# Optimization experiments

Hardware: AMD Instinct MI355X
Metric: run time of the kernel (lower is better)

The kernel has to match this reference:

```python
import jax, jax.numpy as jnp
import numpy as np

NUM_GRAPHS = 512

def setup_inputs() -> dict:
    key = jax.random.key(0)
    ks = jax.random.split(key, 16)
    N, E, F_IN, D = 50000, 800000, 128, 64
    x = jax.random.normal(ks[0], (N, F_IN), dtype=jnp.float32)
    edge_index = jax.random.randint(ks[1], (2, E), 0, N, dtype=jnp.int32)
    batch_index = jnp.sort(jax.random.randint(ks[2], (N,), 0, NUM_GRAPHS, dtype=jnp.int32))
    def lin(k, fin, fout):
        s = 1.0 / np.sqrt(fin)
        return jax.random.uniform(k, (fin, fout), jnp.float32, -s, s)
    return {
        "x": x, "edge_index": edge_index, "batch_index": batch_index,
        "W0": lin(ks[3], F_IN, D), "b0": jnp.zeros((D,), jnp.float32),
        "W1": lin(ks[4], D, D), "b1": jnp.zeros((D,), jnp.float32),
        "W2": lin(ks[5], D, D), "b2": jnp.zeros((D,), jnp.float32),
        "W3": lin(ks[6], D, D), "b3": jnp.zeros((D,), jnp.float32),
        "Wout": lin(ks[7], 2 * D, 1), "bout": jnp.zeros((1,), jnp.float32),
    }

def _gcn_edges(edge_index, N):
    # add self-loops and compute symmetric normalization D^-1/2 (A+I) D^-1/2
    loops = jnp.arange(N, dtype=edge_index.dtype)
    row = jnp.concatenate([edge_index[0], loops])  # source
    col = jnp.concatenate([edge_index[1], loops])  # target
    deg = jax.ops.segment_sum(jnp.ones_like(col, dtype=jnp.float32), col, num_segments=N)
    dinv = jnp.where(deg > 0, jax.lax.rsqrt(deg), 0.0)
    norm = dinv[row] * dinv[col]  # [E+N]
    return row, col, norm

def _gcn_conv(h, row, col, norm, W, b, N):
    h = h @ W                                   # [N, D] linear transform first
    msg = h[row] * norm[:, None]                # gather + scale
    out = jax.ops.segment_sum(msg, col, num_segments=N)  # scatter-add
    return out + b

def reference(x, edge_index, batch_index, W0, b0, W1, b1, W2, b2, W3, b3, Wout, bout):
    N = x.shape[0]
    row, col, norm = _gcn_edges(edge_index, N)
    h = jnp.tanh(_gcn_conv(x, row, col, norm, W0, b0, N))
    h = jnp.tanh(_gcn_conv(h, row, col, norm, W1, b1, N))
    h = jnp.tanh(_gcn_conv(h, row, col, norm, W2, b2, N))
    h = jnp.tanh(_gcn_conv(h, row, col, norm, W3, b3, N))
    gmax = jax.ops.segment_max(h, batch_index, num_segments=NUM_GRAPHS)
    gmax = jnp.where(jnp.isfinite(gmax), gmax, 0.0)  # empty segments -> 0
    gsum = jax.ops.segment_sum(h, batch_index, num_segments=NUM_GRAPHS)
    cnt = jax.ops.segment_sum(jnp.ones((N,), jnp.float32), batch_index, num_segments=NUM_GRAPHS)
    gmean = gsum / jnp.maximum(cnt, 1.0)[:, None]
    hidden = jnp.concatenate([gmax, gmean], axis=1)   # [G, 2D]
    out = hidden @ Wout + bout                        # [G, 1]
    return out, hidden
```

## Files before the change

### kernel.cpp

```cpp
#include <hip/hip_runtime.h>
#include <hip/hip_fp16.h>
#include <math.h>

#define CAP 64
typedef unsigned short ushort_t;
typedef unsigned int uint_t;

__device__ inline float4 f4add(float4 a, float4 b) {
    return make_float4(a.x + b.x, a.y + b.y, a.z + b.z, a.w + b.w);
}

__device__ inline float4 h4tof4(uint2 u) {
    __half2 lo = *reinterpret_cast<__half2*>(&u.x);
    __half2 hi = *reinterpret_cast<__half2*>(&u.y);
    float2 a = __half22float2(lo);
    float2 b = __half22float2(hi);
    return make_float4(a.x, a.y, b.x, b.y);
}

__device__ inline uint_t packh2(float a, float b) {
    __half2 h = __floats2half2_rn(a, b);
    return *reinterpret_cast<uint_t*>(&h);
}

__global__ __launch_bounds__(256) void k_scatter2(const int* __restrict__ row,
                                                  const int* __restrict__ col, int E, int N,
                                                  int* __restrict__ deg, ushort_t* __restrict__ csr) {
    const int part = blockIdx.x & 7;
    const int slot = blockIdx.x >> 3;
    const int nslots = gridDim.x >> 3;
    const int lo = (int)((long long)N * part / 8);
    const int hi = (int)((long long)N * (part + 1) / 8);
    const int nq = E >> 2;
    for (int t = slot * blockDim.x + threadIdx.x; t < nq; t += nslots * blockDim.x) {
        int4 c = ((const int4*)col)[t];
        int4 r = ((const int4*)row)[t];
        if (c.x >= lo && c.x < hi) { int d = atomicAdd(&deg[c.x], 1); if (d < CAP) csr[((size_t)c.x << 6) + d] = (ushort_t)r.x; }
        if (c.y >= lo && c.y < hi) { int d = atomicAdd(&deg[c.y], 1); if (d < CAP) csr[((size_t)c.y << 6) + d] = (ushort_t)r.y; }
        if (c.z >= lo && c.z < hi) { int d = atomicAdd(&deg[c.z], 1); if (d < CAP) csr[((size_t)c.z << 6) + d] = (ushort_t)r.z; }
        if (c.w >= lo && c.w < hi) { int d = atomicAdd(&deg[c.w], 1); if (d < CAP) csr[((size_t)c.w << 6) + d] = (ushort_t)r.w; }
    }
    if (blockIdx.x == 0) {
        for (int e = (nq << 2) + threadIdx.x; e < E; e += blockDim.x) {
            int c = col[e];
            int d = atomicAdd(&deg[c], 1);
            if (d < CAP) csr[((size_t)c << 6) + d] = (ushort_t)row[e];
        }
    }
}

template <int K>
__global__ __launch_bounds__(256) void k_gemm(const float* __restrict__ X,
                                              const float* __restrict__ W,
                                              const int* __restrict__ deg,
                                              ushort_t* __restrict__ Gbh, int N) {
    __shared__ __align__(16) float Wl[32 * 64];
    __shared__ __align__(16) float Xl[64 * 36];

    const int tid = threadIdx.x;
    const int wave = tid >> 6, lane = tid & 63;
    const int d8 = lane & 7, ns = lane >> 3;
    const int n0 = wave * 16 + ns, n1 = n0 + 8;

    const int base = blockIdx.x * 64;
    if (base >= N) return;
    const int tile_n = min(64, N - base);

    float4 a0l = {0,0,0,0}, a0h = {0,0,0,0}, a1l = {0,0,0,0}, a1h = {0,0,0,0};

    for (int kh = 0; kh < K / 32; kh++) {
        __syncthreads();
        for (int i = tid; i < 512; i += 256)
            ((float4*)Wl)[i] = ((const float4*)(W + kh * 2048))[i];
        for (int idx = tid; idx < 512; idx += 256) {
            int n = idx >> 3, q = idx & 7;
            float4 v = {0,0,0,0};
            if (n < tile_n) v = ((const float4*)(X + (size_t)(base + n) * K + kh * 32))[q];
            ((float4*)(Xl + n * 36))[q] = v;
        }
        __syncthreads();

        const float4* xq0 = (const float4*)(Xl + n0 * 36);
        const float4* xq1 = (const float4*)(Xl + n1 * 36);
        const float* wcol = Wl + d8 * 8;
#pragma unroll
        for (int kq = 0; kq < 8; kq++) {
            const float4 x4a = xq0[kq];
            const float4 x4b = xq1[kq];
            const float xs0[4] = {x4a.x, x4a.y, x4a.z, x4a.w};
            const float xs1[4] = {x4b.x, x4b.y, x4b.z, x4b.w};
#pragma unroll
            for (int j = 0; j < 4; j++) {
                const int k = kq * 4 + j;
                const float4 wa = *(const float4*)(wcol + k * 64);
                const float4 wb = *(const float4*)(wcol + k * 64 + 4);
                const float xa = xs0[j];
                const float xb = xs1[j];
                a0l.x = fmaf(xa, wa.x, a0l.x); a0l.y = fmaf(xa, wa.y, a0l.y);
                a0l.z = fmaf(xa, wa.z, a0l.z); a0l.w = fmaf(xa, wa.w, a0l.w);
                a0h.x = fmaf(xa, wb.x, a0h.x); a0h.y = fmaf(xa, wb.y, a0h.y);
                a0h.z = fmaf(xa, wb.z, a0h.z); a0h.w = fmaf(xa, wb.w, a0h.w);
                a1l.x = fmaf(xb, wa.x, a1l.x); a1l.y = fmaf(xb, wa.y, a1l.y);
                a1l.z = fmaf(xb, wa.z, a1l.z); a1l.w = fmaf(xb, wa.w, a1l.w);
                a1h.x = fmaf(xb, wb.x, a1h.x); a1h.y = fmaf(xb, wb.y, a1h.y);
                a1h.z = fmaf(xb, wb.z, a1h.z); a1h.w = fmaf(xb, wb.w, a1h.w);
            }
        }
    }

    int gn0 = base + n0, gn1 = base + n1;
    if (gn0 < N) {
        float s = rsqrtf((float)(deg[gn0] + 1));
        uint4 o;
        o.x = packh2(a0l.x * s, a0l.y * s);
        o.y = packh2(a0l.z * s, a0l.w * s);
        o.z = packh2(a0h.x * s, a0h.y * s);
        o.w = packh2(a0h.z * s, a0h.w * s);
        ((uint4*)(Gbh + (size_t)gn0 * 64))[d8] = o;
    }
    if (gn1 < N) {
        float s = rsqrtf((float)(deg[gn1] + 1));
        uint4 o;
        o.x = packh2(a1l.x * s, a1l.y * s);
        o.y = packh2(a1l.z * s, a1l.w * s);
        o.z = packh2(a1h.x * s, a1h.y * s);
        o.w = packh2(a1h.z * s, a1h.w * s);
        ((uint4*)(Gbh + (size_t)gn1 * 64))[d8] = o;
    }
}

__global__ __launch_bounds__(256) void k_agg(const ushort_t* __restrict__ Gbh,
                                             const int* __restrict__ deg,
                                             const ushort_t* __restrict__ csr,
                                             const float* __restrict__ bias,
                                             float* __restrict__ H, int N) {
    const int tid = threadIdx.x;
    const int wave = tid >> 6, lane = tid & 63;
    const int s = lane >> 4;
    const int q = lane & 15;
    const int n = blockIdx.x * 16 + wave * 4 + s;
    const bool alive = (n < N);

    int cnt = 0;
    if (alive) { cnt = deg[n]; if (cnt > CAP) cnt = CAP; }
    const ushort_t* rowp = csr + ((size_t)(alive ? n : 0) << 6);

    uint4 ia = {0,0,0,0}, ib = {0,0,0,0}, ic = {0,0,0,0}, idd = {0,0,0,0};
    if (cnt > 0)  ia  = *(const uint4*)(rowp);
    if (cnt > 8)  ib  = *(const uint4*)(rowp + 8);
    if (cnt > 16) ic  = *(const uint4*)(rowp + 16);
    if (cnt > 24) idd = *(const uint4*)(rowp + 24);

    float4 acc = {0.f, 0.f, 0.f, 0.f};
    if (alive) acc = h4tof4(((const uint2*)(Gbh + (size_t)n * 64))[q]);

    const uint_t iw[16] = {ia.x, ia.y, ia.z, ia.w, ib.x, ib.y, ib.z, ib.w,
                           ic.x, ic.y, ic.z, ic.w, idd.x, idd.y, idd.z, idd.w};

#pragma unroll
    for (int h = 0; h < 2; h++) {
        const int base = h * 16;
        uint2 hv[16];
#pragma unroll
        for (int m = 0; m < 8; m++) {
            const uint_t u = iw[h * 8 + m];
            const int j0 = u & 0xffff, j1 = u >> 16;
            uint2 a = {0u, 0u}, b = {0u, 0u};
            if (base + 2 * m < cnt)     a = ((const uint2*)(Gbh + (size_t)j0 * 64))[q];
            if (base + 2 * m + 1 < cnt) b = ((const uint2*)(Gbh + (size_t)j1 * 64))[q];
            hv[2 * m] = a;
            hv[2 * m + 1] = b;
        }
        float4 t0 = f4add(h4tof4(hv[0]),  h4tof4(hv[1]));
        float4 t1 = f4add(h4tof4(hv[2]),  h4tof4(hv[3]));
        float4 t2 = f4add(h4tof4(hv[4]),  h4tof4(hv[5]));
        float4 t3 = f4add(h4tof4(hv[6]),  h4tof4(hv[7]));
        float4 t4 = f4add(h4tof4(hv[8]),  h4tof4(hv[9]));
        float4 t5 = f4add(h4tof4(hv[10]), h4tof4(hv[11]));
        float4 t6 = f4add(h4tof4(hv[12]), h4tof4(hv[13]));
        float4 t7 = f4add(h4tof4(hv[14]), h4tof4(hv[15]));
        float4 u0 = f4add(t0, t1), u1 = f4add(t2, t3);
        float4 u2 = f4add(t4, t5), u3 = f4add(t6, t7);
        acc = f4add(acc, f4add(f4add(u0, u1), f4add(u2, u3)));
    }

    for (int i = 32; i < cnt; i += 2) {
        const uint_t u = *(const uint_t*)(rowp + i);
        const int j0 = u & 0xffff;
        acc = f4add(acc, h4tof4(((const uint2*)(Gbh + (size_t)j0 * 64))[q]));
        if (i + 1 < cnt) {
            const int j1 = u >> 16;
            acc = f4add(acc, h4tof4(((const uint2*)(Gbh + (size_t)j1 * 64))[q]));
        }
    }

    if (alive) {
        float dinv = rsqrtf((float)(cnt + 1));
        float4 b4 = ((const float4*)bias)[q];
        float4 r;
        r.x = tanhf(fmaf(acc.x, dinv, b4.x));
        r.y = tanhf(fmaf(acc.y, dinv, b4.y));
        r.z = tanhf(fmaf(acc.z, dinv, b4.z));
        r.w = tanhf(fmaf(acc.w, dinv, b4.w));
        ((float4*)(H + (size_t)n * 64))[q] = r;
    }
}

__global__ __launch_bounds__(256) void k_pool(const float* __restrict__ H,
                                              const int* __restrict__ batch, int N, int Gn,
                                              const float* __restrict__ Wout,
                                              const float* __restrict__ bout,
                                              float* __restrict__ out,
                                              float* __restrict__ hidden) {
    __shared__ float lm[4][64];
    __shared__ float ls[4][64];
    const int g = blockIdx.x;
    if (g >= Gn) return;
    const int tid = threadIdx.x;
    const int w = tid >> 6, lane = tid & 63;

    int lo = 0, hi = N;
    while (lo < hi) { int m = (lo + hi) >> 1; if (batch[m] < g) lo = m + 1; else hi = m; }
    const int s = lo;
    hi = N;
    while (lo < hi) { int m = (lo + hi) >> 1; if (batch[m] < g + 1) lo = m + 1; else hi = m; }
    const int c = lo - s;
    const int e = s + c;

    float m0 = -INFINITY, m1 = -INFINITY, m2 = -INFINITY, m3 = -INFINITY;
    float s0 = 0.f, s1 = 0.f, s2 = 0.f, s3 = 0.f;
    int n = s + w;
    for (; n + 12 < e; n += 16) {
        float v0 = H[(size_t)n * 64 + lane];
        float v1 = H[(size_t)(n + 4) * 64 + lane];
        float v2 = H[(size_t)(n + 8) * 64 + lane];
        float v3 = H[(size_t)(n + 12) * 64 + lane];
        m0 = fmaxf(m0, v0); s0 += v0;
        m1 = fmaxf(m1, v1); s1 += v1;
        m2 = fmaxf(m2, v2); s2 += v2;
        m3 = fmaxf(m3, v3); s3 += v3;
    }
    for (; n < e; n += 4) {
        float v = H[(size_t)n * 64 + lane];
        m0 = fmaxf(m0, v); s0 += v;
    }
    lm[w][lane] = fmaxf(fmaxf(m0, m1), fmaxf(m2, m3));
    ls[w][lane] = (s0 + s1) + (s2 + s3);
    __syncthreads();
    if (w == 0) {
        float vmax = fmaxf(fmaxf(lm[0][lane], lm[1][lane]), fmaxf(lm[2][lane], lm[3][lane]));
        float vsum = (ls[0][lane] + ls[1][lane]) + (ls[2][lane] + ls[3][lane]);
        float gmax = (c > 0) ? vmax : 0.f;
        float gmean = (c > 0) ? vsum / (float)c : 0.f;
        hidden[(size_t)g * 128 + lane] = gmax;
        hidden[(size_t)g * 128 + 64 + lane] = gmean;
        float p = fmaf(gmax, Wout[lane], gmean * Wout[64 + lane]);
        for (int o = 32; o > 0; o >>= 1) p += __shfl_down(p, o);
        if (lane == 0) out[g] = p + bout[0];
    }
}

extern "C" void kernel_launch(void* const* d_in, const int* in_sizes, int n_in,
                              void* d_out, int out_size, void* d_ws, size_t ws_size,
                              hipStream_t stream) {
    const float* x    = (const float*)d_in[0];
    const int*   ei   = (const int*)d_in[1];
    const int*   batch= (const int*)d_in[2];
    const float* W0 = (const float*)d_in[3];  const float* b0 = (const float*)d_in[4];
    const float* W1 = (const float*)d_in[5];  const float* b1 = (const float*)d_in[6];
    const float* W2 = (const float*)d_in[7];  const float* b2 = (const float*)d_in[8];
    const float* W3 = (const float*)d_in[9];  const float* b3 = (const float*)d_in[10];
    const float* Wout = (const float*)d_in[11]; const float* bout = (const float*)d_in[12];

    const int N  = in_sizes[2];
    const int E  = in_sizes[1] / 2;
    const int Gn = out_size / 129;

    const int* row = ei;
    const int* col = ei + E;

    float* out_p    = (float*)d_out;
    float* hidden_p = out_p + Gn;

    char* wp = (char*)d_ws;
    auto alloc = [&](size_t bytes) { void* p = (void*)wp; wp += (bytes + 255) & ~(size_t)255; return p; };
    int*      deg = (int*)alloc((size_t)N * 4);
    ushort_t* csr = (ushort_t*)alloc((size_t)N * CAP * 2);
    ushort_t* Gbh = (ushort_t*)alloc((size_t)N * 64 * 2);
    float*    Hb  = (float*)alloc((size_t)N * 64 * 4);

    hipMemsetAsync(deg, 0, (size_t)N * 4, stream);
    k_scatter2<<<2048, 256, 0, stream>>>(row, col, E, N, deg, csr);

    const int gblocks = (N + 63) / 64;
    const int ablocks = (N + 15) / 16;

    k_gemm<128><<<gblocks, 256, 0, stream>>>(x, W0, deg, Gbh, N);
    k_agg<<<ablocks, 256, 0, stream>>>(Gbh, deg, csr, b0, Hb, N);
    k_gemm<64><<<gblocks, 256, 0, stream>>>(Hb, W1, deg, Gbh, N);
    k_agg<<<ablocks, 256, 0, stream>>>(Gbh, deg, csr, b1, Hb, N);
    k_gemm<64><<<gblocks, 256, 0, stream>>>(Hb, W2, deg, Gbh, N);
    k_agg<<<ablocks, 256, 0, stream>>>(Gbh, deg, csr, b2, Hb, N);
    k_gemm<64><<<gblocks, 256, 0, stream>>>(Hb, W3, deg, Gbh, N);
    k_agg<<<ablocks, 256, 0, stream>>>(Gbh, deg, csr, b3, Hb, N);

    k_pool<<<Gn, 256, 0, stream>>>(Hb, batch, N, Gn, Wout, bout, out_p, hidden_p);
}
```

Before: 274.8 us.

## Fuse aggregation with next layer's linear transform into one kernel

Adds k_agg_gemm, which aggregates neighbour features for 64 nodes, applies bias and tanh, stages the result in shared memory, and multiplies by the next layer's weight to emit the scaled fp16 features. It replaces three agg+gemm kernel pairs, removing the fp32 hidden-state write and re-read between them and three launches. Two ping-pong fp16 buffers are used. In exchange each block now processes 64 nodes with more shared memory (about 33KB), which may lower occupancy for the gather-bound aggregation phase.

```diff
diff --git a/kernel.cpp b/kernel.cpp
--- a/kernel.cpp
+++ b/kernel.cpp
@@ -129,6 +129,150 @@
     }
 }
 
+__global__ __launch_bounds__(256) void k_agg_gemm(const ushort_t* __restrict__ Gin,
+                                                  const int* __restrict__ deg,
+                                                  const ushort_t* __restrict__ csr,
+                                                  const float* __restrict__ bias,
+                                                  const float* __restrict__ W,
+                                                  ushort_t* __restrict__ Gout, int N) {
+    __shared__ __align__(16) float Wl[64 * 64];
+    __shared__ __align__(16) float Hl[64 * 68];
+
+    const int tid = threadIdx.x;
+    const int wave = tid >> 6, lane = tid & 63;
+    const int base = blockIdx.x * 64;
+    if (base >= N) return;
+
+    float4 wreg[4];
+#pragma unroll
+    for (int i = 0; i < 4; i++) wreg[i] = ((const float4*)W)[tid + 256 * i];
+
+    const int s = lane >> 4;
+    const int q = lane & 15;
+
+#pragma unroll
+    for (int r = 0; r < 4; r++) {
+        const int ln = r * 16 + wave * 4 + s;
+        const int n = base + ln;
+        const bool alive = (n < N);
+        int cnt = 0;
+        if (alive) { cnt = deg[n]; if (cnt > CAP) cnt = CAP; }
+        const ushort_t* rowp = csr + ((size_t)(alive ? n : 0) << 6);
+
+        uint4 ia = {0,0,0,0}, ib = {0,0,0,0}, ic = {0,0,0,0}, idd = {0,0,0,0};
+        if (cnt > 0)  ia  = *(const uint4*)(rowp);
+        if (cnt > 8)  ib  = *(const uint4*)(rowp + 8);
+        if (cnt > 16) ic  = *(const uint4*)(rowp + 16);
+        if (cnt > 24) idd = *(const uint4*)(rowp + 24);
+
+        float4 acc = {0.f, 0.f, 0.f, 0.f};
+        if (alive) acc = h4tof4(((const uint2*)(Gin + (size_t)n * 64))[q]);
+
+        const uint_t iw[16] = {ia.x, ia.y, ia.z, ia.w, ib.x, ib.y, ib.z, ib.w,
+                               ic.x, ic.y, ic.z, ic.w, idd.x, idd.y, idd.z, idd.w};
+#pragma unroll
+        for (int h = 0; h < 2; h++) {
+            const int hb = h * 16;
+            uint2 hv[16];
+#pragma unroll
+            for (int m = 0; m < 8; m++) {
+                const uint_t u = iw[h * 8 + m];
+                const int j0 = u & 0xffff, j1 = u >> 16;
+                uint2 a = {0u, 0u}, b = {0u, 0u};
+                if (hb + 2 * m < cnt)     a = ((const uint2*)(Gin + (size_t)j0 * 64))[q];
+                if (hb + 2 * m + 1 < cnt) b = ((const uint2*)(Gin + (size_t)j1 * 64))[q];
+                hv[2 * m] = a;
+                hv[2 * m + 1] = b;
+            }
+            float4 t0 = f4add(h4tof4(hv[0]),  h4tof4(hv[1]));
+            float4 t1 = f4add(h4tof4(hv[2]),  h4tof4(hv[3]));
+            float4 t2 = f4add(h4tof4(hv[4]),  h4tof4(hv[5]));
+            float4 t3 = f4add(h4tof4(hv[6]),  h4tof4(hv[7]));
+            float4 t4 = f4add(h4tof4(hv[8]),  h4tof4(hv[9]));
+            float4 t5 = f4add(h4tof4(hv[10]), h4tof4(hv[11]));
+            float4 t6 = f4add(h4tof4(hv[12]), h4tof4(hv[13]));
+            float4 t7 = f4add(h4tof4(hv[14]), h4tof4(hv[15]));
+            float4 u0 = f4add(t0, t1), u1 = f4add(t2, t3);
+            float4 u2 = f4add(t4, t5), u3 = f4add(t6, t7);
+            acc = f4add(acc, f4add(f4add(u0, u1), f4add(u2, u3)));
+        }
+        for (int i = 32; i < cnt; i += 2) {
+            const uint_t u = *(const uint_t*)(rowp + i);
+            const int j0 = u & 0xffff;
+            acc = f4add(acc, h4tof4(((const uint2*)(Gin + (size_t)j0 * 64))[q]));
+            if (i + 1 < cnt) {
+                const int j1 = u >> 16;
+                acc = f4add(acc, h4tof4(((const uint2*)(Gin + (size_t)j1 * 64))[q]));
+            }
+        }
+
+        float4 r4 = {0.f, 0.f, 0.f, 0.f};
+        if (alive) {
+            float dinv = rsqrtf((float)(cnt + 1));
+            float4 b4 = ((const float4*)bias)[q];
+            r4.x = tanhf(fmaf(acc.x, dinv, b4.x));
+            r4.y = tanhf(fmaf(acc.y, dinv, b4.y));
+            r4.z = tanhf(fmaf(acc.z, dinv, b4.z));
+            r4.w = tanhf(fmaf(acc.w, dinv, b4.w));
+        }
+        ((float4*)(Hl + ln * 68))[q] = r4;
+    }
+
+#pragma unroll
+    for (int i = 0; i < 4; i++) ((float4*)Wl)[tid + 256 * i] = wreg[i];
+    __syncthreads();
+
+    const int d8 = lane & 7, ns = lane >> 3;
+    const int n0 = wave * 16 + ns, n1 = n0 + 8;
+    float4 a0l = {0,0,0,0}, a0h = {0,0,0,0}, a1l = {0,0,0,0}, a1h = {0,0,0,0};
+    const float4* xq0 = (const float4*)(Hl + n0 * 68);
+    const float4* xq1 = (const float4*)(Hl + n1 * 68);
+    const float* wcol = Wl + d8 * 8;
+#pragma unroll
+    for (int kq = 0; kq < 16; kq++) {
+        const float4 x4a = xq0[kq];
+        const float4 x4b = xq1[kq];
+        const float xs0[4] = {x4a.x, x4a.y, x4a.z, x4a.w};
+        const float xs1[4] = {x4b.x, x4b.y, x4b.z, x4b.w};
+#pragma unroll
+        for (int j = 0; j < 4; j++) {
+            const int k = kq * 4 + j;
+            const float4 wa = *(const float4*)(wcol + k * 64);
+            const float4 wb = *(const float4*)(wcol + k * 64 + 4);
+            const float xa = xs0[j];
+            const float xb = xs1[j];
+            a0l.x = fmaf(xa, wa.x, a0l.x); a0l.y = fmaf(xa, wa.y, a0l.y);
+            a0l.z = fmaf(xa, wa.z, a0l.z); a0l.w = fmaf(xa, wa.w, a0l.w);
+            a0h.x = fmaf(xa, wb.x, a0h.x); a0h.y = fmaf(xa, wb.y, a0h.y);
+            a0h.z = fmaf(xa, wb.z, a0h.z); a0h.w = fmaf(xa, wb.w, a0h.w);
+            a1l.x = fmaf(xb, wa.x, a1l.x); a1l.y = fmaf(xb, wa.y, a1l.y);
+            a1l.z = fmaf(xb, wa.z, a1l.z); a1l.w = fmaf(xb, wa.w, a1l.w);
+            a1h.x = fmaf(xb, wb.x, a1h.x); a1h.y = fmaf(xb, wb.y, a1h.y);
+            a1h.z = fmaf(xb, wb.z, a1h.z); a1h.w = fmaf(xb, wb.w, a1h.w);
+        }
+    }
+
+    int gn0 = base + n0, gn1 = base + n1;
+    if (gn0 < N) {
+        float sc = rsqrtf((float)(deg[gn0] + 1));
+        uint4 o;
+        o.x = packh2(a0l.x * sc, a0l.y * sc);
+        o.y = packh2(a0l.z * sc, a0l.w * sc);
+        o.z = packh2(a0h.x * sc, a0h.y * sc);
+        o.w = packh2(a0h.z * sc, a0h.w * sc);
+        ((uint4*)(Gout + (size_t)gn0 * 64))[d8] = o;
+    }
+    if (gn1 < N) {
+        float sc = rsqrtf((float)(deg[gn1] + 1));
+        uint4 o;
+        o.x = packh2(a1l.x * sc, a1l.y * sc);
+        o.y = packh2(a1l.z * sc, a1l.w * sc);
+        o.z = packh2(a1h.x * sc, a1h.y * sc);
+        o.w = packh2(a1h.z * sc, a1h.w * sc);
+        ((uint4*)(Gout + (size_t)gn1 * 64))[d8] = o;
+    }
+}
+
 __global__ __launch_bounds__(256) void k_agg(const ushort_t* __restrict__ Gbh,
                                              const int* __restrict__ deg,
                                              const ushort_t* __restrict__ csr,
@@ -159,15 +303,15 @@
 
 #pragma unroll
     for (int h = 0; h < 2; h++) {
-        const int base = h * 16;
+        const int hb = h * 16;
         uint2 hv[16];
 #pragma unroll
         for (int m = 0; m < 8; m++) {
             const uint_t u = iw[h * 8 + m];
             const int j0 = u & 0xffff, j1 = u >> 16;
             uint2 a = {0u, 0u}, b = {0u, 0u};
-            if (base + 2 * m < cnt)     a = ((const uint2*)(Gbh + (size_t)j0 * 64))[q];
-            if (base + 2 * m + 1 < cnt) b = ((const uint2*)(Gbh + (size_t)j1 * 64))[q];
+            if (hb + 2 * m < cnt)     a = ((const uint2*)(Gbh + (size_t)j0 * 64))[q];
+            if (hb + 2 * m + 1 < cnt) b = ((const uint2*)(Gbh + (size_t)j1 * 64))[q];
             hv[2 * m] = a;
             hv[2 * m + 1] = b;
         }
@@ -286,7 +430,8 @@
     auto alloc = [&](size_t bytes) { void* p = (void*)wp; wp += (bytes + 255) & ~(size_t)255; return p; };
     int*      deg = (int*)alloc((size_t)N * 4);
     ushort_t* csr = (ushort_t*)alloc((size_t)N * CAP * 2);
-    ushort_t* Gbh = (ushort_t*)alloc((size_t)N * 64 * 2);
+    ushort_t* Ga  = (ushort_t*)alloc((size_t)N * 64 * 2);
+    ushort_t* Gc  = (ushort_t*)alloc((size_t)N * 64 * 2);
     float*    Hb  = (float*)alloc((size_t)N * 64 * 4);
 
     hipMemsetAsync(deg, 0, (size_t)N * 4, stream);
@@ -295,14 +440,11 @@
     const int gblocks = (N + 63) / 64;
     const int ablocks = (N + 15) / 16;
 
-    k_gemm<128><<<gblocks, 256, 0, stream>>>(x, W0, deg, Gbh, N);
-    k_agg<<<ablocks, 256, 0, stream>>>(Gbh, deg, csr, b0, Hb, N);
-    k_gemm<64><<<gblocks, 256, 0, stream>>>(Hb, W1, deg, Gbh, N);
-    k_agg<<<ablocks, 256, 0, stream>>>(Gbh, deg, csr, b1, Hb, N);
-    k_gemm<64><<<gblocks, 256, 0, stream>>>(Hb, W2, deg, Gbh, N);
-    k_agg<<<ablocks, 256, 0, stream>>>(Gbh, deg, csr, b2, Hb, N);
-    k_gemm<64><<<gblocks, 256, 0, stream>>>(Hb, W3, deg, Gbh, N);
-    k_agg<<<ablocks, 256, 0, stream>>>(Gbh, deg, csr, b3, Hb, N);
+    k_gemm<128><<<gblocks, 256, 0, stream>>>(x, W0, deg, Ga, N);
+    k_agg_gemm<<<gblocks, 256, 0, stream>>>(Ga, deg, csr, b0, W1, Gc, N);
+    k_agg_gemm<<<gblocks, 256, 0, stream>>>(Gc, deg, csr, b1, W2, Ga, N);
+    k_agg_gemm<<<gblocks, 256, 0, stream>>>(Ga, deg, csr, b2, W3, Gc, N);
+    k_agg<<<ablocks, 256, 0, stream>>>(Gc, deg, csr, b3, Hb, N);
 
     k_pool<<<Gn, 256, 0, stream>>>(Hb, batch, N, Gn, Wout, bout, out_p, hidden_p);
 }
```

After: 543.9 us. 1.98x slower.
